# Performance work log

Measured on AMD Instinct MI355X. Metric: run time of the kernel, lower is better.

The kernel has to match this reference:

```python
import jax, jax.numpy as jnp
import numpy as np

N = 100000
E = 1000000
IN_F, HID, NCLS = 128, 128, 40
EPS = 1e-5


def _gconv(h, src, dst, W, b):
    # DGL GraphConv with norm='both', allow_zero_in_degree=True (degrees clamped to >=1).
    ones = jnp.ones(src.shape, jnp.float32)
    dout = jnp.clip(jax.ops.segment_sum(ones, src, num_segments=N), 1.0)   # out-degree of src nodes
    din = jnp.clip(jax.ops.segment_sum(ones, dst, num_segments=N), 1.0)    # in-degree of dst nodes
    x = (h * jax.lax.rsqrt(dout)[:, None]) @ W            # [N, out] matmul-first (linear commutes with sum-aggregation)
    y = jax.ops.segment_sum(x[src], dst, num_segments=N)  # SpMM: scatter-add over edges
    y = y * jax.lax.rsqrt(din)[:, None]
    return y + b if b is not None else y


def _bn(h, gamma, beta):
    # BatchNorm1d training-mode math over the node dimension (biased variance).
    m = jnp.mean(h, axis=0)
    v = jnp.mean(jnp.square(h - m), axis=0)
    return (h - m) * jax.lax.rsqrt(v + EPS) * gamma + beta


def setup_inputs() -> dict:
    key = jax.random.key(0)
    ks = jax.random.split(key, 16)
    feat = jax.random.normal(ks[0], (N, IN_F), jnp.float32)
    src0 = jax.random.randint(ks[1], (E,), 0, N, jnp.int32)
    dst0 = jax.random.randint(ks[2], (E,), 0, N, jnp.int32)
    src1 = jax.random.randint(ks[3], (E,), 0, N, jnp.int32)
    dst1 = jax.random.randint(ks[4], (E,), 0, N, jnp.int32)
    order_attn = jax.random.uniform(ks[5], (2,), jnp.float32)
    s = lambda d_in, d_out: 1.0 / np.sqrt(d_in)
    W0 = jax.random.uniform(ks[6], (IN_F, HID), jnp.float32, -s(IN_F, HID), s(IN_F, HID))
    W1 = jax.random.uniform(ks[7], (HID, HID), jnp.float32, -s(HID, HID), s(HID, HID))
    W2 = jax.random.uniform(ks[8], (HID, NCLS), jnp.float32, -s(HID, NCLS), s(HID, NCLS))
    b2 = jnp.zeros((NCLS,), jnp.float32)
    L0 = jax.random.uniform(ks[9], (IN_F, HID), jnp.float32, -s(IN_F, HID), s(IN_F, HID))
    L1 = jax.random.uniform(ks[10], (HID, HID), jnp.float32, -s(HID, HID), s(HID, HID))
    L2 = jax.random.uniform(ks[11], (HID, NCLS), jnp.float32, -s(HID, NCLS), s(HID, NCLS))
    gamma0 = jnp.ones((HID,), jnp.float32); beta0 = jnp.zeros((HID,), jnp.float32)
    gamma1 = jnp.ones((HID,), jnp.float32); beta1 = jnp.zeros((HID,), jnp.float32)
    return dict(feat=feat, src0=src0, dst0=dst0, src1=src1, dst1=dst1, order_attn=order_attn,
                W0=W0, W1=W1, W2=W2, b2=b2, L0=L0, L1=L1, L2=L2,
                gamma0=gamma0, beta0=beta0, gamma1=gamma1, beta1=beta1)


def reference(feat, src0, dst0, src1, dst1, order_attn, W0, W1, W2, b2, L0, L1, L2,
              gamma0, beta0, gamma1, beta1):
    # Multi-graph path (len(graph)==2, n_layers==3, use_linear=True); dropout = identity (eval).
    h = feat
    # layer 0: order_attn-weighted combination of two adjacency variants
    conv1 = _gconv(h, src0, dst0, W0, None)
    conv2 = _gconv(h, src1, dst1, W0, None)
    conv = order_attn[0] * conv1 + order_attn[1] * conv2
    h = conv + h @ L0
    h = jax.nn.relu(_bn(h, gamma0, beta0))
    # layer 1 (convs[-2]) on graph[0]
    h = _gconv(h, src0, dst0, W1, None) + h @ L1
    h = jax.nn.relu(_bn(h, gamma1, beta1))
    # layer 2 (convs[-1]) on graph[0], with bias
    h = _gconv(h, src0, dst0, W2, b2) + h @ L2
    return h
```

## Files before the change

kernel.cpp:

```cpp
#include <hip/hip_runtime.h>
#include <math.h>

#define N_NODES 100000
#define N_EDGES 1000000
#define F 128
#define NC 40
#define BN_EPS 1e-5f
#define CH 32
#define EC (N_EDGES / CH)
#define WIN0 65536
#define NB1 (N_NODES - WIN0)
#define PROW (N_NODES / 4)

typedef unsigned int uint;
typedef unsigned short ushort;
typedef __attribute__((ext_vector_type(8))) short vbf8;
typedef __attribute__((ext_vector_type(4))) float vf4;

__device__ __forceinline__ float bf_lo(uint v) { return __uint_as_float(v << 16); }
__device__ __forceinline__ float bf_hi(uint v) { return __uint_as_float(v & 0xffff0000u); }
__device__ __forceinline__ ushort f2bf(float f) {
  uint u = __float_as_uint(f);
  u = u + 0x7fffu + ((u >> 16) & 1u);
  return (ushort)(u >> 16);
}
__device__ __forceinline__ uint pk2(float a, float b) {
  return (uint)f2bf(a) | ((uint)f2bf(b) << 16);
}

__global__ __launch_bounds__(256) void hist_count_k(
    const int* __restrict__ s0, const int* __restrict__ d0,
    const int* __restrict__ s1, const int* __restrict__ d1,
    unsigned* __restrict__ partial) {
  __shared__ unsigned bins[16384];
  int c = blockIdx.x, w = blockIdx.y, a = blockIdx.z;
  const int* keys = (a == 0) ? s0 : (a == 1) ? d0 : (a == 2) ? s1 : d1;
  int base = w * WIN0;
  int nb = w ? NB1 : WIN0;
  int nwords = nb >> 2;
  int t = threadIdx.x;
  for (int i = t; i < nwords; i += 256) bins[i] = 0;
  __syncthreads();
  int e0 = c * EC;
  for (int e = e0 + t; e < e0 + EC; e += 256) {
    int b = keys[e] - base;
    if ((unsigned)b < (unsigned)nb)
      atomicAdd(&bins[b >> 2], 1u << ((b & 3) * 8));
  }
  __syncthreads();
  unsigned* dst = partial + (size_t)(a * CH + c) * PROW + (w ? (WIN0 >> 2) : 0);
  for (int i = t; i < nwords; i += 256) dst[i] = bins[i];
}

__global__ __launch_bounds__(256) void deg_reduce_k(
    unsigned* __restrict__ partial, float* __restrict__ rs4, ushort* __restrict__ rsO01u,
    int* __restrict__ degIn0, int* __restrict__ degIn1,
    float* __restrict__ st0, float* __restrict__ st1) {
  int word = blockIdx.x * 256 + threadIdx.x;
  if (blockIdx.y == 0 && word < 256) { st0[word] = 0.f; st1[word] = 0.f; }
  if (word >= PROW) return;
  int a = blockIdx.y;
  bool din = (a == 1) || (a == 3);
  unsigned r0 = 0, r1 = 0, r2 = 0, r3 = 0;
  unsigned* rowp = partial + (size_t)a * CH * PROW + word;
  for (int c = 0; c < CH; ++c) {
    unsigned* p = rowp + (size_t)c * PROW;
    unsigned v = *p;
    if (din) *p = r0 | (r1 << 8) | (r2 << 16) | (r3 << 24);
    r0 += v & 255u; r1 += (v >> 8) & 255u; r2 += (v >> 16) & 255u; r3 += (v >> 24) & 255u;
  }
  int b = word * 4;
  float4 r;
  r.x = rsqrtf((float)max(r0, 1u));
  r.y = rsqrtf((float)max(r1, 1u));
  r.z = rsqrtf((float)max(r2, 1u));
  r.w = rsqrtf((float)max(r3, 1u));
  *(float4*)&rs4[(size_t)a * N_NODES + b] = r;
  if (a == 0) {
    rsO01u[2 * (b + 0)] = f2bf(r.x); rsO01u[2 * (b + 1)] = f2bf(r.y);
    rsO01u[2 * (b + 2)] = f2bf(r.z); rsO01u[2 * (b + 3)] = f2bf(r.w);
  }
  if (a == 2) {
    rsO01u[2 * (b + 0) + 1] = f2bf(r.x); rsO01u[2 * (b + 1) + 1] = f2bf(r.y);
    rsO01u[2 * (b + 2) + 1] = f2bf(r.z); rsO01u[2 * (b + 3) + 1] = f2bf(r.w);
  }
  if (a == 1) { degIn0[b] = r0; degIn0[b + 1] = r1; degIn0[b + 2] = r2; degIn0[b + 3] = r3; }
  if (a == 3) { degIn1[b] = r0; degIn1[b + 1] = r1; degIn1[b + 2] = r2; degIn1[b + 3] = r3; }
}

__global__ void scan_local_k(const int* __restrict__ cnt0, const int* __restrict__ cnt1,
                             int* __restrict__ out0, int* __restrict__ out1,
                             int* __restrict__ bsum) {
  __shared__ int lds[256];
  const int* cnt = blockIdx.y ? cnt1 : cnt0;
  int* out = blockIdx.y ? out1 : out0;
  int base = blockIdx.x * 2048;
  int t = threadIdx.x;
  int v[8];
  int s = 0;
#pragma unroll
  for (int j = 0; j < 8; ++j) {
    int idx = base + t * 8 + j;
    v[j] = (idx < N_NODES) ? cnt[idx] : 0;
    s += v[j];
  }
  lds[t] = s;
  __syncthreads();
  for (int off = 1; off < 256; off <<= 1) {
    int x = (t >= off) ? lds[t - off] : 0;
    __syncthreads();
    lds[t] += x;
    __syncthreads();
  }
  int excl = lds[t] - s;
  if (t == 255) bsum[blockIdx.y * 64 + blockIdx.x] = lds[255];
  int run = excl;
#pragma unroll
  for (int j = 0; j < 8; ++j) {
    int idx = base + t * 8 + j;
    if (idx < N_NODES) out[idx] = run;
    run += v[j];
  }
}

__global__ void scan_top_k(int* bsum, int nb) {
  int w = threadIdx.x >> 6, t = threadIdx.x & 63;
  int* b = bsum + w * 64;
  int orig = (t < nb) ? b[t] : 0;
  int v = orig;
  for (int off = 1; off < 64; off <<= 1) {
    int u = __shfl_up(v, off);
    if (t >= off) v += u;
  }
  if (t < nb) b[t] = v - orig;
}

__global__ void scan_apply_k(int* __restrict__ rp0, int* __restrict__ rp1,
                             const int* __restrict__ bsum) {
  int* rp = blockIdx.y ? rp1 : rp0;
  const int* bs = bsum + blockIdx.y * 64;
  int i = blockIdx.x * 256 + threadIdx.x;
  if (i < N_NODES) rp[i] += bs[i >> 11];
  if (i == 0) rp[N_NODES] = N_EDGES;
}

__global__ __launch_bounds__(256) void csr_fill2_k(
    const int* __restrict__ src0, const int* __restrict__ dst0, const int* __restrict__ rp0g,
    int* __restrict__ csr0g,
    const int* __restrict__ src1, const int* __restrict__ dst1, const int* __restrict__ rp1g,
    int* __restrict__ csr1g, const unsigned* __restrict__ partial) {
  __shared__ unsigned bins[16384];
  int c = blockIdx.x, w = blockIdx.y, g = blockIdx.z;
  const int* src = g ? src1 : src0;
  const int* dst = g ? dst1 : dst0;
  const int* rp = g ? rp1g : rp0g;
  int* csr = g ? csr1g : csr0g;
  int aIdx = g ? 3 : 1;
  int base = w * WIN0;
  int nb = w ? NB1 : WIN0;
  int nwords = nb >> 2;
  const unsigned* sp = partial + (size_t)(aIdx * CH + c) * PROW + (w ? (WIN0 >> 2) : 0);
  int t = threadIdx.x;
  for (int i = t; i < nwords; i += 256) bins[i] = sp[i];
  __syncthreads();
  int e0 = c * EC;
  for (int e = e0 + t; e < e0 + EC; e += 256) {
    int d = dst[e];
    int b = d - base;
    if ((unsigned)b < (unsigned)nb) {
      int sh = (b & 3) * 8;
      unsigned old = atomicAdd(&bins[b >> 2], 1u << sh);
      int off = (old >> sh) & 255;
      csr[rp[d] + off] = src[e];
    }
  }
}

__global__ __launch_bounds__(256) void pack_all_k(
    const float* __restrict__ x, uint* __restrict__ y,
    const float* __restrict__ Wa, const float* __restrict__ Wb,
    const float* __restrict__ Wc, const float* __restrict__ Wd,
    ushort* __restrict__ pk) {
  int b = blockIdx.x;
  int t = threadIdx.x;
  if (b < 1024) {
    size_t total = (size_t)N_NODES * F / 8;
    for (size_t idx = b * 256 + t; idx < total; idx += (size_t)1024 * 256) {
      float4 v1 = ((const float4*)x)[idx * 2];
      float4 v2 = ((const float4*)x)[idx * 2 + 1];
      uint4 o;
      o.x = pk2(v1.x, v1.y);
      o.y = pk2(v1.z, v1.w);
      o.z = pk2(v2.x, v2.y);
      o.w = pk2(v2.z, v2.w);
      ((uint4*)y)[idx] = o;
    }
  } else {
    int bb = b - 1024;
    int m = bb >> 3;
    int idx = (bb & 7) * 256 + t;
    const float* W = (m == 0) ? Wa : (m == 1) ? Wb : (m == 2) ? Wc : Wd;
    int lane = idx & 63;
    int nt = (idx >> 6) & 7;
    int ks = idx >> 9;
    int j = (lane & 15) + nt * 16;
    int kb = (lane >> 4) * 8 + ks * 32;
    ushort v[8];
#pragma unroll
    for (int q = 0; q < 8; ++q) v[q] = f2bf(W[(size_t)(kb + q) * F + j]);
    *(uint4*)(pk + (size_t)m * 16384 + (size_t)idx * 8) = *(uint4*)v;
  }
}

__device__ __forceinline__ void acc8(uint4 v, float c, float* a) {
  a[0] = fmaf(bf_lo(v.x), c, a[0]); a[1] = fmaf(bf_hi(v.x), c, a[1]);
  a[2] = fmaf(bf_lo(v.y), c, a[2]); a[3] = fmaf(bf_hi(v.y), c, a[3]);
  a[4] = fmaf(bf_lo(v.z), c, a[4]); a[5] = fmaf(bf_hi(v.z), c, a[5]);
  a[6] = fmaf(bf_lo(v.w), c, a[6]); a[7] = fmaf(bf_hi(v.w), c, a[7]);
}

__device__ __forceinline__ void gather_run(const int* __restrict__ p, int n, float w,
                                           const float* __restrict__ rsO,
                                           const uint4* __restrict__ xr, int l, float* a) {
  int e = 0;
  for (; e + 3 < n; e += 4) {
    int s0 = p[e], s1 = p[e + 1], s2 = p[e + 2], s3 = p[e + 3];
    float c0 = w * rsO[s0], c1 = w * rsO[s1];
    float c2 = w * rsO[s2], c3 = w * rsO[s3];
    uint4 v0 = xr[(size_t)s0 * 16 + l];
    uint4 v1 = xr[(size_t)s1 * 16 + l];
    uint4 v2 = xr[(size_t)s2 * 16 + l];
    uint4 v3 = xr[(size_t)s3 * 16 + l];
    acc8(v0, c0, a); acc8(v1, c1, a); acc8(v2, c2, a); acc8(v3, c3, a);
  }
  for (; e < n; ++e) {
    int s = p[e];
    float c = w * rsO[s];
    uint4 v = xr[(size_t)s * 16 + l];
    acc8(v, c, a);
  }
}

__global__ __launch_bounds__(256) void gather_dual_q_k(
    const uint* __restrict__ xbf, const float* __restrict__ attn,
    const float* __restrict__ rsO0f, const float* __restrict__ rsO1f,
    const float* __restrict__ rsI0, const int* __restrict__ rp0, const int* __restrict__ csr0,
    const float* __restrict__ rsI1, const int* __restrict__ rp1, const int* __restrict__ csr1,
    uint* __restrict__ outbf) {
  int node = blockIdx.x * 16 + (threadIdx.x >> 4);
  int l = threadIdx.x & 15;
  int b0 = rp0[node], n0 = rp0[node + 1] - b0;
  int b1 = rp1[node], n1 = rp1[node + 1] - b1;
  float w0 = attn[0] * rsI0[node];
  float w1 = attn[1] * rsI1[node];
  const uint4* xr = (const uint4*)xbf;
  float a[8] = {0.f, 0.f, 0.f, 0.f, 0.f, 0.f, 0.f, 0.f};
  gather_run(csr0 + b0, n0, w0, rsO0f, xr, l, a);
  gather_run(csr1 + b1, n1, w1, rsO1f, xr, l, a);
  uint4 o;
  o.x = pk2(a[0], a[1]); o.y = pk2(a[2], a[3]);
  o.z = pk2(a[4], a[5]); o.w = pk2(a[6], a[7]);
  ((uint4*)outbf)[(size_t)node * 16 + l] = o;
}

__device__ __forceinline__ void accbn(uint4 v, float c, const float* sc, const float* sh,
                                      float* a) {
  a[0] = fmaf(fmaxf(fmaf(bf_lo(v.x), sc[0], sh[0]), 0.f), c, a[0]);
  a[1] = fmaf(fmaxf(fmaf(bf_hi(v.x), sc[1], sh[1]), 0.f), c, a[1]);
  a[2] = fmaf(fmaxf(fmaf(bf_lo(v.y), sc[2], sh[2]), 0.f), c, a[2]);
  a[3] = fmaf(fmaxf(fmaf(bf_hi(v.y), sc[3], sh[3]), 0.f), c, a[3]);
  a[4] = fmaf(fmaxf(fmaf(bf_lo(v.z), sc[4], sh[4]), 0.f), c, a[4]);
  a[5] = fmaf(fmaxf(fmaf(bf_hi(v.z), sc[5], sh[5]), 0.f), c, a[5]);
  a[6] = fmaf(fmaxf(fmaf(bf_lo(v.w), sc[6], sh[6]), 0.f), c, a[6]);
  a[7] = fmaf(fmaxf(fmaf(bf_hi(v.w), sc[7], sh[7]), 0.f), c, a[7]);
}

__global__ __launch_bounds__(256) void gather_bn_q_k(
    const uint* __restrict__ xbf, const float* __restrict__ st,
    const float* __restrict__ gamma, const float* __restrict__ beta,
    const float* __restrict__ rsO,
    const float* __restrict__ rsI, const int* __restrict__ rp, const int* __restrict__ csr,
    uint* __restrict__ outbf) {
  int node = blockIdx.x * 16 + (threadIdx.x >> 4);
  int l = threadIdx.x & 15;
  float sc[8], sh[8];
#pragma unroll
  for (int j = 0; j < 8; ++j) {
    int c = 8 * l + j;
    float m = st[c] * (1.f / (float)N_NODES);
    float v = st[128 + c] * (1.f / (float)N_NODES) - m * m;
    float s = gamma[c] * rsqrtf(fmaxf(v, 0.f) + BN_EPS);
    sc[j] = s;
    sh[j] = beta[c] - m * s;
  }
  int b0 = rp[node], T = rp[node + 1] - b0;
  const int* p = csr + b0;
  const uint4* xr = (const uint4*)xbf;
  float a[8] = {0.f, 0.f, 0.f, 0.f, 0.f, 0.f, 0.f, 0.f};
  int e = 0;
  for (; e + 1 < T; e += 2) {
    int s0 = p[e], s1 = p[e + 1];
    float c0 = rsO[s0], c1 = rsO[s1];
    uint4 v0 = xr[(size_t)s0 * 16 + l];
    uint4 v1 = xr[(size_t)s1 * 16 + l];
    accbn(v0, c0, sc, sh, a);
    accbn(v1, c1, sc, sh, a);
  }
  if (e < T) {
    int s0 = p[e];
    float c0 = rsO[s0];
    uint4 v0 = xr[(size_t)s0 * 16 + l];
    accbn(v0, c0, sc, sh, a);
  }
  float sd = rsI[node];
  uint4 o;
  o.x = pk2(a[0] * sd, a[1] * sd); o.y = pk2(a[2] * sd, a[3] * sd);
  o.z = pk2(a[4] * sd, a[5] * sd); o.w = pk2(a[6] * sd, a[7] * sd);
  ((uint4*)outbf)[(size_t)node * 16 + l] = o;
}

__global__ void gather40_add_k(const uint* __restrict__ x2bf, const float* __restrict__ rsI,
                               const int* __restrict__ rp, const int* __restrict__ csr,
                               float* __restrict__ out) {
  int node = (blockIdx.x * 256 + threadIdx.x) >> 5;
  int lane = threadIdx.x & 31;
  if (node >= N_NODES || lane >= 20) return;
  float l = 0.f, h = 0.f;
  int e = rp[node], end = rp[node + 1];
  for (; e + 3 < end; e += 4) {
    int sA = csr[e], sB = csr[e + 1], sC = csr[e + 2], sD = csr[e + 3];
    uint vA = x2bf[(size_t)sA * 20 + lane];
    uint vB = x2bf[(size_t)sB * 20 + lane];
    uint vC = x2bf[(size_t)sC * 20 + lane];
    uint vD = x2bf[(size_t)sD * 20 + lane];
    l += (bf_lo(vA) + bf_lo(vB)) + (bf_lo(vC) + bf_lo(vD));
    h += (bf_hi(vA) + bf_hi(vB)) + (bf_hi(vC) + bf_hi(vD));
  }
  for (; e < end; ++e) {
    uint vA = x2bf[(size_t)csr[e] * 20 + lane];
    l += bf_lo(vA);
    h += bf_hi(vA);
  }
  float sd = rsI[node];
  float2 p = *(float2*)(out + (size_t)node * NC + lane * 2);
  *(float2*)(out + (size_t)node * NC + lane * 2) = make_float2(p.x + l * sd, p.y + h * sd);
}

__global__ __launch_bounds__(256) void gemm_mfma_k(
    const ushort* __restrict__ A1, const ushort* __restrict__ A2,
    const ushort* __restrict__ pkA, const ushort* __restrict__ pkB,
    float* __restrict__ st, ushort* __restrict__ Cb) {
  __shared__ float sst[256];
  int t = threadIdx.x;
  int wave = t >> 6, lane = t & 63;
  int kgrp = lane >> 4, lrow = lane & 15;
  int arow = blockIdx.x * 64 + wave * 16 + lrow;
  bool rok = arow < N_NODES;
  const vbf8* a1p = (const vbf8*)(A1 + (size_t)(rok ? arow : 0) * F);
  const vbf8* a2p = (const vbf8*)(A2 + (size_t)(rok ? arow : 0) * F);
  const vbf8* wap = (const vbf8*)pkA + lane;
  const vbf8* wbp = (const vbf8*)pkB + lane;
  sst[t] = 0.f;
  __syncthreads();
  vbf8 zero = {0, 0, 0, 0, 0, 0, 0, 0};
  vf4 acc[8];
#pragma unroll
  for (int i = 0; i < 8; ++i) acc[i] = (vf4){0.f, 0.f, 0.f, 0.f};
#pragma unroll
  for (int ks = 0; ks < 4; ++ks) {
    vbf8 a1 = rok ? a1p[ks * 4 + kgrp] : zero;
    vbf8 a2 = rok ? a2p[ks * 4 + kgrp] : zero;
#pragma unroll
    for (int nt = 0; nt < 8; ++nt)
      acc[nt] = __builtin_amdgcn_mfma_f32_16x16x32_bf16(a1, wap[(ks * 8 + nt) * 64], acc[nt], 0, 0, 0);
#pragma unroll
    for (int nt = 0; nt < 8; ++nt)
      acc[nt] = __builtin_amdgcn_mfma_f32_16x16x32_bf16(a2, wbp[(ks * 8 + nt) * 64], acc[nt], 0, 0, 0);
  }
  int rbase = blockIdx.x * 64 + wave * 16 + kgrp * 4;
#pragma unroll
  for (int nt = 0; nt < 8; ++nt) {
    int col = nt * 16 + lrow;
#pragma unroll
    for (int r = 0; r < 4; ++r) {
      int row = rbase + r;
      if (row < N_NODES) Cb[(size_t)row * F + col] = f2bf(acc[nt][r]);
    }
  }
#pragma unroll
  for (int nt = 0; nt < 8; ++nt) {
    float s = acc[nt][0] + acc[nt][1] + acc[nt][2] + acc[nt][3];
    float q = acc[nt][0] * acc[nt][0] + acc[nt][1] * acc[nt][1] +
              acc[nt][2] * acc[nt][2] + acc[nt][3] * acc[nt][3];
    s += __shfl_xor(s, 16); q += __shfl_xor(q, 16);
    s += __shfl_xor(s, 32); q += __shfl_xor(q, 32);
    if (lane < 16) {
      atomicAdd(&sst[nt * 16 + lane], s);
      atomicAdd(&sst[128 + nt * 16 + lane], q);
    }
  }
  __syncthreads();
  atomicAdd(&st[t], sst[t]);
}

__global__ __launch_bounds__(256) void gemm_mfma_bn_k(
    const ushort* __restrict__ A1, const ushort* __restrict__ A2,
    const float* __restrict__ stin, const float* __restrict__ gamma,
    const float* __restrict__ beta,
    const ushort* __restrict__ pkA, const ushort* __restrict__ pkB,
    float* __restrict__ st, ushort* __restrict__ Cb) {
  __shared__ float sst[256];
  __shared__ float scl[128], shl[128];
  int t = threadIdx.x;
  int wave = t >> 6, lane = t & 63;
  int kgrp = lane >> 4, lrow = lane & 15;
  int arow = blockIdx.x * 64 + wave * 16 + lrow;
  bool rok = arow < N_NODES;
  if (t < 128) {
    float m = stin[t] * (1.f / (float)N_NODES);
    float v = stin[128 + t] * (1.f / (float)N_NODES) - m * m;
    float s = gamma[t] * rsqrtf(fmaxf(v, 0.f) + BN_EPS);
    scl[t] = s;
    shl[t] = beta[t] - m * s;
  }
  const vbf8* a1p = (const vbf8*)(A1 + (size_t)(rok ? arow : 0) * F);
  const vbf8* a2p = (const vbf8*)(A2 + (size_t)(rok ? arow : 0) * F);
  const vbf8* wap = (const vbf8*)pkA + lane;
  const vbf8* wbp = (const vbf8*)pkB + lane;
  sst[t] = 0.f;
  __syncthreads();
  vbf8 zero = {0, 0, 0, 0, 0, 0, 0, 0};
  vf4 acc[8];
#pragma unroll
  for (int i = 0; i < 8; ++i) acc[i] = (vf4){0.f, 0.f, 0.f, 0.f};
#pragma unroll
  for (int ks = 0; ks < 4; ++ks) {
    vbf8 a1 = rok ? a1p[ks * 4 + kgrp] : zero;
    vbf8 a2 = zero;
    if (rok) {
      vbf8 a2r = a2p[ks * 4 + kgrp];
      const float* scp = &scl[ks * 32 + kgrp * 8];
      const float* shp = &shl[ks * 32 + kgrp * 8];
      ushort o[8];
#pragma unroll
      for (int q = 0; q < 8; ++q) {
        float f = __uint_as_float(((uint)(ushort)a2r[q]) << 16);
        f = fmaxf(fmaf(f, scp[q], shp[q]), 0.f);
        o[q] = f2bf(f);
      }
      a2 = *(vbf8*)o;
    }
#pragma unroll
    for (int nt = 0; nt < 8; ++nt)
      acc[nt] = __builtin_amdgcn_mfma_f32_16x16x32_bf16(a1, wap[(ks * 8 + nt) * 64], acc[nt], 0, 0, 0);
#pragma unroll
    for (int nt = 0; nt < 8; ++nt)
      acc[nt] = __builtin_amdgcn_mfma_f32_16x16x32_bf16(a2, wbp[(ks * 8 + nt) * 64], acc[nt], 0, 0, 0);
  }
  int rbase = blockIdx.x * 64 + wave * 16 + kgrp * 4;
#pragma unroll
  for (int nt = 0; nt < 8; ++nt) {
    int col = nt * 16 + lrow;
#pragma unroll
    for (int r = 0; r < 4; ++r) {
      int row = rbase + r;
      if (row < N_NODES) Cb[(size_t)row * F + col] = f2bf(acc[nt][r]);
    }
  }
#pragma unroll
  for (int nt = 0; nt < 8; ++nt) {
    float s = acc[nt][0] + acc[nt][1] + acc[nt][2] + acc[nt][3];
    float q = acc[nt][0] * acc[nt][0] + acc[nt][1] * acc[nt][1] +
              acc[nt][2] * acc[nt][2] + acc[nt][3] * acc[nt][3];
    s += __shfl_xor(s, 16); q += __shfl_xor(q, 16);
    s += __shfl_xor(s, 32); q += __shfl_xor(q, 32);
    if (lane < 16) {
      atomicAdd(&sst[nt * 16 + lane], s);
      atomicAdd(&sst[128 + nt * 16 + lane], q);
    }
  }
  __syncthreads();
  atomicAdd(&st[t], sst[t]);
}

__global__ __launch_bounds__(256) void gemm40_dual_k(
    const uint* __restrict__ h1b, const float* __restrict__ st,
    const float* __restrict__ gamma, const float* __restrict__ beta,
    const float* __restrict__ W2, const float* __restrict__ L2, const float* __restrict__ bias,
    const float* __restrict__ rsO, uint* __restrict__ x2bf, float* __restrict__ outp) {
  __shared__ float Alds[25 * 128];
  __shared__ float Wl[128 * NC];
  __shared__ float Ll[128 * NC];
  __shared__ float scl[128], shl[128];
  int t = threadIdx.x;
  int r0 = blockIdx.x * 25;
  if (t < 128) {
    float m = st[t] / (float)N_NODES;
    float v = st[128 + t] / (float)N_NODES - m * m;
    float s = gamma[t] * rsqrtf(fmaxf(v, 0.f) + BN_EPS);
    scl[t] = s;
    shl[t] = beta[t] - m * s;
  }
  __syncthreads();
#pragma unroll
  for (int p = 0; p < 4; ++p) {
    int flat = t * 4 + p * 1024;
    if (flat < 25 * 128) {
      int lrr = flat >> 7, k = flat & 127;
      int row = r0 + lrr;
      float4 v = make_float4(0.f, 0.f, 0.f, 0.f);
      if (row < N_NODES) {
        uint2 u = *(const uint2*)(h1b + (size_t)row * 64 + (k >> 1));
        v = make_float4(bf_lo(u.x), bf_hi(u.x), bf_lo(u.y), bf_hi(u.y));
      }
      float4 scv = *(float4*)&scl[k];
      float4 shv = *(float4*)&shl[k];
      v.x = fmaxf(fmaf(v.x, scv.x, shv.x), 0.f);
      v.y = fmaxf(fmaf(v.y, scv.y, shv.y), 0.f);
      v.z = fmaxf(fmaf(v.z, scv.z, shv.z), 0.f);
      v.w = fmaxf(fmaf(v.w, scv.w, shv.w), 0.f);
      *(float4*)&Alds[flat] = v;
    }
  }
#pragma unroll
  for (int p = 0; p < 5; ++p) {
    int flat = t * 4 + p * 1024;
    if (flat < 128 * NC) {
      *(float4*)&Wl[flat] = *(const float4*)(W2 + flat);
      *(float4*)&Ll[flat] = *(const float4*)(L2 + flat);
    }
  }
  __syncthreads();
  if (t < 250) {
    int lrr = t / 10, cg = t % 10;
    float w0 = 0.f, w1 = 0.f, w2 = 0.f, w3 = 0.f;
    float l0 = 0.f, l1 = 0.f, l2 = 0.f, l3 = 0.f;
#pragma unroll 8
    for (int k = 0; k < 128; ++k) {
      float a = Alds[lrr * 128 + k];
      float4 w = *(float4*)&Wl[k * NC + cg * 4];
      float4 l = *(float4*)&Ll[k * NC + cg * 4];
      w0 = fmaf(a, w.x, w0); w1 = fmaf(a, w.y, w1);
      w2 = fmaf(a, w.z, w2); w3 = fmaf(a, w.w, w3);
      l0 = fmaf(a, l.x, l0); l1 = fmaf(a, l.y, l1);
      l2 = fmaf(a, l.z, l2); l3 = fmaf(a, l.w, l3);
    }
    int row = r0 + lrr;
    if (row < N_NODES) {
      float s = rsO[row];
      uint2 xo = make_uint2(pk2(w0 * s, w1 * s), pk2(w2 * s, w3 * s));
      *(uint2*)(x2bf + (size_t)row * 20 + cg * 2) = xo;
      float4 bv = *(const float4*)(bias + cg * 4);
      float4 oo = make_float4(l0 + bv.x, l1 + bv.y, l2 + bv.z, l3 + bv.w);
      *(float4*)(outp + (size_t)row * NC + cg * 4) = oo;
    }
  }
}

extern "C" void kernel_launch(void* const* d_in, const int* in_sizes, int n_in,
                              void* d_out, int out_size, void* d_ws, size_t ws_size,
                              hipStream_t stream) {
  const float* feat = (const float*)d_in[0];
  const int* src0 = (const int*)d_in[1];
  const int* dst0 = (const int*)d_in[2];
  const int* src1 = (const int*)d_in[3];
  const int* dst1 = (const int*)d_in[4];
  const float* attn = (const float*)d_in[5];
  const float* W0 = (const float*)d_in[6];
  const float* W1 = (const float*)d_in[7];
  const float* W2 = (const float*)d_in[8];
  const float* b2 = (const float*)d_in[9];
  const float* L0 = (const float*)d_in[10];
  const float* L1 = (const float*)d_in[11];
  const float* L2 = (const float*)d_in[12];
  const float* gamma0 = (const float*)d_in[13];
  const float* beta0 = (const float*)d_in[14];
  const float* gamma1 = (const float*)d_in[15];
  const float* beta1 = (const float*)d_in[16];
  float* out = (float*)d_out;

  char* base = (char*)d_ws;
  size_t off = 0;
  auto alloc = [&](size_t bytes) -> void* {
    void* p = base + off;
    off += (bytes + 255) & ~(size_t)255;
    return p;
  };
  unsigned* partial = (unsigned*)alloc((size_t)4 * CH * PROW * 4);
  float* rs4 = (float*)alloc(4 * (size_t)N_NODES * 4);
  uint* rsO01 = (uint*)alloc((size_t)N_NODES * 4);
  int* degIn0 = (int*)alloc(N_NODES * 4);
  int* degIn1 = (int*)alloc(N_NODES * 4);
  int* rp0 = (int*)alloc((N_NODES + 1) * 4);
  int* rp1 = (int*)alloc((N_NODES + 1) * 4);
  int* bsum = (int*)alloc(128 * 4);
  int* csr0 = (int*)alloc((size_t)N_EDGES * 4);
  int* csr1 = (int*)alloc((size_t)N_EDGES * 4);
  float* st0 = (float*)alloc(256 * 4);
  float* st1 = (float*)alloc(256 * 4);
  ushort* wpk = (ushort*)alloc((size_t)4 * 16384 * 2);
  uint* featbf = (uint*)alloc((size_t)N_NODES * 64 * 4);
  uint* aggbf = (uint*)alloc((size_t)N_NODES * 64 * 4);
  uint* hrow = (uint*)alloc((size_t)N_NODES * 64 * 4);
  uint* g1buf = (uint*)alloc((size_t)N_NODES * 64 * 4);
  if (off > ws_size) return;

  uint* x2bf = featbf;

  float* rs_out0 = rs4;
  float* rs_in0 = rs4 + N_NODES;
  float* rs_out1 = rs4 + 2 * N_NODES;
  float* rs_in1 = rs4 + 3 * N_NODES;

  hist_count_k<<<dim3(CH, 2, 4), 256, 0, stream>>>(src0, dst0, src1, dst1, partial);
  deg_reduce_k<<<dim3((PROW + 255) / 256, 4), 256, 0, stream>>>(
      partial, rs4, (ushort*)rsO01, degIn0, degIn1, st0, st1);
  const int SCB = (N_NODES + 2047) / 2048;
  scan_local_k<<<dim3(SCB, 2), 256, 0, stream>>>(degIn0, degIn1, rp0, rp1, bsum);
  scan_top_k<<<1, 128, 0, stream>>>(bsum, SCB);
  scan_apply_k<<<dim3((N_NODES + 255) / 256, 2), 256, 0, stream>>>(rp0, rp1, bsum);
  csr_fill2_k<<<dim3(CH, 2, 2), 256, 0, stream>>>(src0, dst0, rp0, csr0,
                                                  src1, dst1, rp1, csr1, partial);

  pack_all_k<<<1056, 256, 0, stream>>>(feat, featbf, W0, L0, W1, L1, wpk);

  const int GB = (N_NODES + 63) / 64;

  gather_dual_q_k<<<N_NODES / 16, 256, 0, stream>>>(featbf, attn, rs_out0, rs_out1,
                                                    rs_in0, rp0, csr0,
                                                    rs_in1, rp1, csr1, aggbf);
  gemm_mfma_k<<<GB, 256, 0, stream>>>((ushort*)aggbf, (ushort*)featbf, wpk, wpk + 16384,
                                      st0, (ushort*)hrow);

  gather_bn_q_k<<<N_NODES / 16, 256, 0, stream>>>(hrow, st0, gamma0, beta0, rs_out0,
                                                  rs_in0, rp0, csr0, g1buf);
  gemm_mfma_bn_k<<<GB, 256, 0, stream>>>((ushort*)g1buf, (ushort*)hrow, st0, gamma0, beta0,
                                         wpk + 2 * 16384, wpk + 3 * 16384, st1, (ushort*)hrow);

  gemm40_dual_k<<<(N_NODES + 24) / 25, 256, 0, stream>>>(hrow, st1, gamma1, beta1, W2, L2, b2,
                                                         rs_out0, x2bf, out);
  gather40_add_k<<<(N_NODES * 32 + 255) / 256, 256, 0, stream>>>(x2bf, rs_in0, rp0, csr0, out);
}
```

Before: 492.5 us.

## Fuse SpMM gathers into MFMA GEMM kernels via LDS-staged A tiles

Merges the neighbor-gather kernels into the following MFMA GEMM kernels for layers 0 and 1. Each block gathers the aggregated rows for its 64 nodes into padded shared memory and feeds them straight to the MFMA loop. This removes the aggregated-feature buffer write and reread and cuts two launches. In exchange, each block now does 4 nodes per 16-lane group serially, so there is less parallelism and latency hiding in the gather phase, plus extra LDS use that may lower occupancy. Layer 1 output now goes to a separate buffer instead of being written in place.

Result: no change. 489.8 us (-0.5%).

```diff
diff --git a/kernel.cpp b/kernel.cpp
--- a/kernel.cpp
+++ b/kernel.cpp
@@ -11,6 +11,7 @@
 #define WIN0 65536
 #define NB1 (N_NODES - WIN0)
 #define PROW (N_NODES / 4)
+#define ALD 66
 
 typedef unsigned int uint;
 typedef unsigned short ushort;
@@ -241,28 +242,6 @@
   }
 }
 
-__global__ __launch_bounds__(256) void gather_dual_q_k(
-    const uint* __restrict__ xbf, const float* __restrict__ attn,
-    const float* __restrict__ rsO0f, const float* __restrict__ rsO1f,
-    const float* __restrict__ rsI0, const int* __restrict__ rp0, const int* __restrict__ csr0,
-    const float* __restrict__ rsI1, const int* __restrict__ rp1, const int* __restrict__ csr1,
-    uint* __restrict__ outbf) {
-  int node = blockIdx.x * 16 + (threadIdx.x >> 4);
-  int l = threadIdx.x & 15;
-  int b0 = rp0[node], n0 = rp0[node + 1] - b0;
-  int b1 = rp1[node], n1 = rp1[node + 1] - b1;
-  float w0 = attn[0] * rsI0[node];
-  float w1 = attn[1] * rsI1[node];
-  const uint4* xr = (const uint4*)xbf;
-  float a[8] = {0.f, 0.f, 0.f, 0.f, 0.f, 0.f, 0.f, 0.f};
-  gather_run(csr0 + b0, n0, w0, rsO0f, xr, l, a);
-  gather_run(csr1 + b1, n1, w1, rsO1f, xr, l, a);
-  uint4 o;
-  o.x = pk2(a[0], a[1]); o.y = pk2(a[2], a[3]);
-  o.z = pk2(a[4], a[5]); o.w = pk2(a[6], a[7]);
-  ((uint4*)outbf)[(size_t)node * 16 + l] = o;
-}
-
 __device__ __forceinline__ void accbn(uint4 v, float c, const float* sc, const float* sh,
                                       float* a) {
   a[0] = fmaf(fmaxf(fmaf(bf_lo(v.x), sc[0], sh[0]), 0.f), c, a[0]);
@@ -273,50 +252,6 @@
   a[5] = fmaf(fmaxf(fmaf(bf_hi(v.z), sc[5], sh[5]), 0.f), c, a[5]);
   a[6] = fmaf(fmaxf(fmaf(bf_lo(v.w), sc[6], sh[6]), 0.f), c, a[6]);
   a[7] = fmaf(fmaxf(fmaf(bf_hi(v.w), sc[7], sh[7]), 0.f), c, a[7]);
-}
-
-__global__ __launch_bounds__(256) void gather_bn_q_k(
-    const uint* __restrict__ xbf, const float* __restrict__ st,
-    const float* __restrict__ gamma, const float* __restrict__ beta,
-    const float* __restrict__ rsO,
-    const float* __restrict__ rsI, const int* __restrict__ rp, const int* __restrict__ csr,
-    uint* __restrict__ outbf) {
-  int node = blockIdx.x * 16 + (threadIdx.x >> 4);
-  int l = threadIdx.x & 15;
-  float sc[8], sh[8];
-#pragma unroll
-  for (int j = 0; j < 8; ++j) {
-    int c = 8 * l + j;
-    float m = st[c] * (1.f / (float)N_NODES);
-    float v = st[128 + c] * (1.f / (float)N_NODES) - m * m;
-    float s = gamma[c] * rsqrtf(fmaxf(v, 0.f) + BN_EPS);
-    sc[j] = s;
-    sh[j] = beta[c] - m * s;
-  }
-  int b0 = rp[node], T = rp[node + 1] - b0;
-  const int* p = csr + b0;
-  const uint4* xr = (const uint4*)xbf;
-  float a[8] = {0.f, 0.f, 0.f, 0.f, 0.f, 0.f, 0.f, 0.f};
-  int e = 0;
-  for (; e + 1 < T; e += 2) {
-    int s0 = p[e], s1 = p[e + 1];
-    float c0 = rsO[s0], c1 = rsO[s1];
-    uint4 v0 = xr[(size_t)s0 * 16 + l];
-    uint4 v1 = xr[(size_t)s1 * 16 + l];
-    accbn(v0, c0, sc, sh, a);
-    accbn(v1, c1, sc, sh, a);
-  }
-  if (e < T) {
-    int s0 = p[e];
-    float c0 = rsO[s0];
-    uint4 v0 = xr[(size_t)s0 * 16 + l];
-    accbn(v0, c0, sc, sh, a);
-  }
-  float sd = rsI[node];
-  uint4 o;
-  o.x = pk2(a[0] * sd, a[1] * sd); o.y = pk2(a[2] * sd, a[3] * sd);
-  o.z = pk2(a[4] * sd, a[5] * sd); o.w = pk2(a[6] * sd, a[7] * sd);
-  ((uint4*)outbf)[(size_t)node * 16 + l] = o;
 }
 
 __global__ void gather40_add_k(const uint* __restrict__ x2bf, const float* __restrict__ rsI,
@@ -346,29 +281,53 @@
   *(float2*)(out + (size_t)node * NC + lane * 2) = make_float2(p.x + l * sd, p.y + h * sd);
 }
 
-__global__ __launch_bounds__(256) void gemm_mfma_k(
-    const ushort* __restrict__ A1, const ushort* __restrict__ A2,
+__global__ __launch_bounds__(256) void gemm_g_mfma_k(
+    const uint* __restrict__ xbf, const float* __restrict__ attn,
+    const float* __restrict__ rsO0f, const float* __restrict__ rsO1f,
+    const float* __restrict__ rsI0, const int* __restrict__ rp0, const int* __restrict__ csr0,
+    const float* __restrict__ rsI1, const int* __restrict__ rp1, const int* __restrict__ csr1,
     const ushort* __restrict__ pkA, const ushort* __restrict__ pkB,
     float* __restrict__ st, ushort* __restrict__ Cb) {
+  __shared__ uint Alds[64 * ALD];
   __shared__ float sst[256];
   int t = threadIdx.x;
+  sst[t] = 0.f;
+  {
+    int g = t >> 4, l = t & 15;
+    const uint4* xr = (const uint4*)xbf;
+    float w0 = attn[0], w1 = attn[1];
+#pragma unroll
+    for (int i = 0; i < 4; ++i) {
+      int ln = g * 4 + i;
+      int node = blockIdx.x * 64 + ln;
+      float a[8] = {0.f, 0.f, 0.f, 0.f, 0.f, 0.f, 0.f, 0.f};
+      if (node < N_NODES) {
+        int b0 = rp0[node], n0 = rp0[node + 1] - b0;
+        int b1 = rp1[node], n1 = rp1[node + 1] - b1;
+        gather_run(csr0 + b0, n0, w0 * rsI0[node], rsO0f, xr, l, a);
+        gather_run(csr1 + b1, n1, w1 * rsI1[node], rsO1f, xr, l, a);
+      }
+      uint4 o;
+      o.x = pk2(a[0], a[1]); o.y = pk2(a[2], a[3]);
+      o.z = pk2(a[4], a[5]); o.w = pk2(a[6], a[7]);
+      *(uint4*)&Alds[ln * ALD + l * 4] = o;
+    }
+  }
+  __syncthreads();
   int wave = t >> 6, lane = t & 63;
   int kgrp = lane >> 4, lrow = lane & 15;
   int arow = blockIdx.x * 64 + wave * 16 + lrow;
   bool rok = arow < N_NODES;
-  const vbf8* a1p = (const vbf8*)(A1 + (size_t)(rok ? arow : 0) * F);
-  const vbf8* a2p = (const vbf8*)(A2 + (size_t)(rok ? arow : 0) * F);
+  const vbf8* a2p = (const vbf8*)((const ushort*)xbf + (size_t)(rok ? arow : 0) * F);
   const vbf8* wap = (const vbf8*)pkA + lane;
   const vbf8* wbp = (const vbf8*)pkB + lane;
-  sst[t] = 0.f;
-  __syncthreads();
   vbf8 zero = {0, 0, 0, 0, 0, 0, 0, 0};
   vf4 acc[8];
 #pragma unroll
   for (int i = 0; i < 8; ++i) acc[i] = (vf4){0.f, 0.f, 0.f, 0.f};
 #pragma unroll
   for (int ks = 0; ks < 4; ++ks) {
-    vbf8 a1 = rok ? a1p[ks * 4 + kgrp] : zero;
+    vbf8 a1 = *(const vbf8*)&Alds[(wave * 16 + lrow) * ALD + (ks * 4 + kgrp) * 4];
     vbf8 a2 = rok ? a2p[ks * 4 + kgrp] : zero;
 #pragma unroll
     for (int nt = 0; nt < 8; ++nt)
@@ -403,19 +362,19 @@
   atomicAdd(&st[t], sst[t]);
 }
 
-__global__ __launch_bounds__(256) void gemm_mfma_bn_k(
-    const ushort* __restrict__ A1, const ushort* __restrict__ A2,
+__global__ __launch_bounds__(256) void gemm_g_bn_k(
+    const uint* __restrict__ xbf,
     const float* __restrict__ stin, const float* __restrict__ gamma,
     const float* __restrict__ beta,
+    const float* __restrict__ rsO,
+    const float* __restrict__ rsI, const int* __restrict__ rp, const int* __restrict__ csr,
     const ushort* __restrict__ pkA, const ushort* __restrict__ pkB,
     float* __restrict__ st, ushort* __restrict__ Cb) {
+  __shared__ uint Alds[64 * ALD];
   __shared__ float sst[256];
   __shared__ float scl[128], shl[128];
   int t = threadIdx.x;
-  int wave = t >> 6, lane = t & 63;
-  int kgrp = lane >> 4, lrow = lane & 15;
-  int arow = blockIdx.x * 64 + wave * 16 + lrow;
-  bool rok = arow < N_NODES;
+  sst[t] = 0.f;
   if (t < 128) {
     float m = stin[t] * (1.f / (float)N_NODES);
     float v = stin[128 + t] * (1.f / (float)N_NODES) - m * m;
@@ -423,19 +382,60 @@
     scl[t] = s;
     shl[t] = beta[t] - m * s;
   }
-  const vbf8* a1p = (const vbf8*)(A1 + (size_t)(rok ? arow : 0) * F);
-  const vbf8* a2p = (const vbf8*)(A2 + (size_t)(rok ? arow : 0) * F);
+  __syncthreads();
+  {
+    int g = t >> 4, l = t & 15;
+    const uint4* xr = (const uint4*)xbf;
+    float sc[8], sh[8];
+#pragma unroll
+    for (int j = 0; j < 8; ++j) { sc[j] = scl[8 * l + j]; sh[j] = shl[8 * l + j]; }
+#pragma unroll
+    for (int i = 0; i < 4; ++i) {
+      int ln = g * 4 + i;
+      int node = blockIdx.x * 64 + ln;
+      float a[8] = {0.f, 0.f, 0.f, 0.f, 0.f, 0.f, 0.f, 0.f};
+      float sd = 0.f;
+      if (node < N_NODES) {
+        sd = rsI[node];
+        int b0 = rp[node], T = rp[node + 1] - b0;
+        const int* p = csr + b0;
+        int e = 0;
+        for (; e + 1 < T; e += 2) {
+          int s0 = p[e], s1 = p[e + 1];
+          float c0 = rsO[s0], c1 = rsO[s1];
+          uint4 v0 = xr[(size_t)s0 * 16 + l];
+          uint4 v1 = xr[(size_t)s1 * 16 + l];
+          accbn(v0, c0, sc, sh, a);
+          accbn(v1, c1, sc, sh, a);
+        }
+        if (e < T) {
+          int s0 = p[e];
+          float c0 = rsO[s0];
+          uint4 v0 = xr[(size_t)s0 * 16 + l];
+          accbn(v0, c0, sc, sh, a);
+        }
+      }
+      uint4 o;
+      o.x = pk2(a[0] * sd, a[1] * sd); o.y = pk2(a[2] * sd, a[3] * sd);
+      o.z = pk2(a[4] * sd, a[5] * sd); o.w = pk2(a[6] * sd, a[7] * sd);
+      *(uint4*)&Alds[ln * ALD + l * 4] = o;
+    }
+  }
+  __syncthreads();
+  int wave = t >> 6, lane = t & 63;
+  int kgrp = lane >> 4, lrow = lane & 15;
+  int arow = blockIdx.x * 64 + wave * 16 + lrow;
+  bool rok = arow < N_NODES;
+  const vbf8* a2p = (const vbf8*)((const ushort*)xbf + (size_t)(rok ? arow : 0) * F);
   const vbf8* wap = (const vbf8*)pkA + lane;
   const vbf8* wbp = (const vbf8*)pkB + lane;
-  sst[t] = 0.f;
-  __syncthreads();
   vbf8 zero = {0, 0, 0, 0, 0, 0, 0, 0};
   vf4 acc[8];
 #pragma unroll
   for (int i = 0; i < 8; ++i) acc[i] = (vf4){0.f, 0.f, 0.f, 0.f};
 #pragma unroll
   for (int ks = 0; ks < 4; ++ks) {
-    vbf8 a1 = rok ? a1p[ks * 4 + kgrp] : zero;
+    vbf8 a1 = *(const vbf8*)&Alds[(wave * 16 + lrow) * ALD + (ks * 4 + kgrp) * 4];
     vbf8 a2 = zero;
     if (rok) {
       vbf8 a2r = a2p[ks * 4 + kgrp];
@@ -600,7 +600,6 @@
   float* st1 = (float*)alloc(256 * 4);
   ushort* wpk = (ushort*)alloc((size_t)4 * 16384 * 2);
   uint* featbf = (uint*)alloc((size_t)N_NODES * 64 * 4);
-  uint* aggbf = (uint*)alloc((size_t)N_NODES * 64 * 4);
   uint* hrow = (uint*)alloc((size_t)N_NODES * 64 * 4);
   uint* g1buf = (uint*)alloc((size_t)N_NODES * 64 * 4);
   if (off > ws_size) return;
@@ -626,18 +625,15 @@
 
   const int GB = (N_NODES + 63) / 64;
 
-  gather_dual_q_k<<<N_NODES / 16, 256, 0, stream>>>(featbf, attn, rs_out0, rs_out1,
-                                                    rs_in0, rp0, csr0,
-                                                    rs_in1, rp1, csr1, aggbf);
-  gemm_mfma_k<<<GB, 256, 0, stream>>>((ushort*)aggbf, (ushort*)featbf, wpk, wpk + 16384,
-                                      st0, (ushort*)hrow);
-
-  gather_bn_q_k<<<N_NODES / 16, 256, 0, stream>>>(hrow, st0, gamma0, beta0, rs_out0,
-                                                  rs_in0, rp0, csr0, g1buf);
-  gemm_mfma_bn_k<<<GB, 256, 0, stream>>>((ushort*)g1buf, (ushort*)hrow, st0, gamma0, beta0,
-                                         wpk + 2 * 16384, wpk + 3 * 16384, st1, (ushort*)hrow);
-
-  gemm40_dual_k<<<(N_NODES + 24) / 25, 256, 0, stream>>>(hrow, st1, gamma1, beta1, W2, L2, b2,
+  gemm_g_mfma_k<<<GB, 256, 0, stream>>>(featbf, attn, rs_out0, rs_out1,
+                                        rs_in0, rp0, csr0, rs_in1, rp1, csr1,
+                                        wpk, wpk + 16384, st0, (ushort*)hrow);
+
+  gemm_g_bn_k<<<GB, 256, 0, stream>>>(hrow, st0, gamma0, beta0, rs_out0,
+                                      rs_in0, rp0, csr0,
+                                      wpk + 2 * 16384, wpk + 3 * 16384, st1, (ushort*)g1buf);
+
+  gemm40_dual_k<<<(N_NODES + 24) / 25, 256, 0, stream>>>(g1buf, st1, gamma1, beta1, W2, L2, b2,
                                                          rs_out0, x2bf, out);
   gather40_add_k<<<(N_NODES * 32 + 255) / 256, 256, 0, stream>>>(x2bf, rs_in0, rp0, csr0, out);
 }
```

## Stage GEMM outputs in LDS for coalesced stores; replace BN-stat atomics with two-stage reduction

Applied to the files above, without the earlier changes.

Both MFMA GEMM kernels now pack pairs of bf16 results through a lane shuffle into a padded LDS tile, then write each 64-row block with coalesced 16-byte stores instead of scattered 2-byte stores. The per-block BatchNorm sum and sum-of-squares partials are written to a per-block buffer rather than atomically added into one 256-float array. Two small kernels then reduce those partials deterministically. This removes global atomic contention and uncoalesced writes, at the cost of extra LDS use, two more launches per layer, and an extra partial buffer.

New measurement: 468.1 us. -5.0%, faster.

```diff
diff --git a/kernel.cpp b/kernel.cpp
--- a/kernel.cpp
+++ b/kernel.cpp
@@ -11,6 +11,8 @@
 #define WIN0 65536
 #define NB1 (N_NODES - WIN0)
 #define PROW (N_NODES / 4)
+#define CSU 68
+#define GB 1563
 
 typedef unsigned int uint;
 typedef unsigned short ushort;
@@ -54,10 +56,8 @@
 
 __global__ __launch_bounds__(256) void deg_reduce_k(
     unsigned* __restrict__ partial, float* __restrict__ rs4, ushort* __restrict__ rsO01u,
-    int* __restrict__ degIn0, int* __restrict__ degIn1,
-    float* __restrict__ st0, float* __restrict__ st1) {
+    int* __restrict__ degIn0, int* __restrict__ degIn1) {
   int word = blockIdx.x * 256 + threadIdx.x;
-  if (blockIdx.y == 0 && word < 256) { st0[word] = 0.f; st1[word] = 0.f; }
   if (word >= PROW) return;
   int a = blockIdx.y;
   bool din = (a == 1) || (a == 3);
@@ -210,6 +210,22 @@
     for (int q = 0; q < 8; ++q) v[q] = f2bf(W[(size_t)(kb + q) * F + j]);
     *(uint4*)(pk + (size_t)m * 16384 + (size_t)idx * 8) = *(uint4*)v;
   }
+}
+
+__global__ void st_part_k(const float* __restrict__ stm, float* __restrict__ stp, int ncopies) {
+  int b = blockIdx.x, t = threadIdx.x;
+  int lo = b * 25, hi = min(ncopies, lo + 25);
+  float s = 0.f;
+  for (int k = lo; k < hi; ++k) s += stm[(size_t)k * 256 + t];
+  stp[b * 256 + t] = s;
+}
+
+__global__ void st_final_k(const float* __restrict__ stp, float* __restrict__ st) {
+  int t = threadIdx.x;
+  float s = 0.f;
+#pragma unroll
+  for (int k = 0; k < 64; ++k) s += stp[k * 256 + t];
+  st[t] = s;
 }
 
 __device__ __forceinline__ void acc8(uint4 v, float c, float* a) {
@@ -349,9 +365,12 @@
 __global__ __launch_bounds__(256) void gemm_mfma_k(
     const ushort* __restrict__ A1, const ushort* __restrict__ A2,
     const ushort* __restrict__ pkA, const ushort* __restrict__ pkB,
-    float* __restrict__ st, ushort* __restrict__ Cb) {
+    float* __restrict__ stm, ushort* __restrict__ Cb) {
+  __shared__ uint Cl[64 * CSU];
   __shared__ float sst[256];
   int t = threadIdx.x;
+  sst[t] = 0.f;
+  __syncthreads();
   int wave = t >> 6, lane = t & 63;
   int kgrp = lane >> 4, lrow = lane & 15;
   int arow = blockIdx.x * 64 + wave * 16 + lrow;
@@ -360,8 +379,6 @@
   const vbf8* a2p = (const vbf8*)(A2 + (size_t)(rok ? arow : 0) * F);
   const vbf8* wap = (const vbf8*)pkA + lane;
   const vbf8* wbp = (const vbf8*)pkB + lane;
-  sst[t] = 0.f;
-  __syncthreads();
   vbf8 zero = {0, 0, 0, 0, 0, 0, 0, 0};
   vf4 acc[8];
 #pragma unroll
@@ -377,14 +394,14 @@
     for (int nt = 0; nt < 8; ++nt)
       acc[nt] = __builtin_amdgcn_mfma_f32_16x16x32_bf16(a2, wbp[(ks * 8 + nt) * 64], acc[nt], 0, 0, 0);
   }
-  int rbase = blockIdx.x * 64 + wave * 16 + kgrp * 4;
+  int row_l = wave * 16 + kgrp * 4;
 #pragma unroll
   for (int nt = 0; nt < 8; ++nt) {
-    int col = nt * 16 + lrow;
 #pragma unroll
     for (int r = 0; r < 4; ++r) {
-      int row = rbase + r;
-      if (row < N_NODES) Cb[(size_t)row * F + col] = f2bf(acc[nt][r]);
+      float w = acc[nt][r];
+      float o = __shfl_xor(w, 1);
+      if ((lrow & 1) == 0) Cl[(row_l + r) * CSU + nt * 8 + (lrow >> 1)] = pk2(w, o);
     }
   }
 #pragma unroll
@@ -400,7 +417,15 @@
     }
   }
   __syncthreads();
-  atomicAdd(&st[t], sst[t]);
+#pragma unroll
+  for (int i = 0; i < 4; ++i) {
+    int u = t + 256 * i;
+    int row = u >> 4, seg = (u & 15) * 4;
+    int grow = blockIdx.x * 64 + row;
+    if (grow < N_NODES)
+      *(uint4*)((uint*)Cb + (size_t)grow * 64 + seg) = *(uint4*)&Cl[row * CSU + seg];
+  }
+  stm[(size_t)blockIdx.x * 256 + t] = sst[t];
 }
 
 __global__ __launch_bounds__(256) void gemm_mfma_bn_k(
@@ -408,14 +433,12 @@
     const float* __restrict__ stin, const float* __restrict__ gamma,
     const float* __restrict__ beta,
     const ushort* __restrict__ pkA, const ushort* __restrict__ pkB,
-    float* __restrict__ st, ushort* __restrict__ Cb) {
+    float* __restrict__ stm, ushort* __restrict__ Cb) {
+  __shared__ uint Cl[64 * CSU];
   __shared__ float sst[256];
   __shared__ float scl[128], shl[128];
   int t = threadIdx.x;
-  int wave = t >> 6, lane = t & 63;
-  int kgrp = lane >> 4, lrow = lane & 15;
-  int arow = blockIdx.x * 64 + wave * 16 + lrow;
-  bool rok = arow < N_NODES;
+  sst[t] = 0.f;
   if (t < 128) {
     float m = stin[t] * (1.f / (float)N_NODES);
     float v = stin[128 + t] * (1.f / (float)N_NODES) - m * m;
@@ -423,12 +446,15 @@
     scl[t] = s;
     shl[t] = beta[t] - m * s;
   }
+  __syncthreads();
+  int wave = t >> 6, lane = t & 63;
+  int kgrp = lane >> 4, lrow = lane & 15;
+  int arow = blockIdx.x * 64 + wave * 16 + lrow;
+  bool rok = arow < N_NODES;
   const vbf8* a1p = (const vbf8*)(A1 + (size_t)(rok ? arow : 0) * F);
   const vbf8* a2p = (const vbf8*)(A2 + (size_t)(rok ? arow : 0) * F);
   const vbf8* wap = (const vbf8*)pkA + lane;
   const vbf8* wbp = (const vbf8*)pkB + lane;
-  sst[t] = 0.f;
-  __syncthreads();
   vbf8 zero = {0, 0, 0, 0, 0, 0, 0, 0};
   vf4 acc[8];
 #pragma unroll
@@ -457,14 +483,14 @@
     for (int nt = 0; nt < 8; ++nt)
       acc[nt] = __builtin_amdgcn_mfma_f32_16x16x32_bf16(a2, wbp[(ks * 8 + nt) * 64], acc[nt], 0, 0, 0);
   }
-  int rbase = blockIdx.x * 64 + wave * 16 + kgrp * 4;
+  int row_l = wave * 16 + kgrp * 4;
 #pragma unroll
   for (int nt = 0; nt < 8; ++nt) {
-    int col = nt * 16 + lrow;
 #pragma unroll
     for (int r = 0; r < 4; ++r) {
-      int row = rbase + r;
-      if (row < N_NODES) Cb[(size_t)row * F + col] = f2bf(acc[nt][r]);
+      float w = acc[nt][r];
+      float o = __shfl_xor(w, 1);
+      if ((lrow & 1) == 0) Cl[(row_l + r) * CSU + nt * 8 + (lrow >> 1)] = pk2(w, o);
     }
   }
 #pragma unroll
@@ -480,7 +506,15 @@
     }
   }
   __syncthreads();
-  atomicAdd(&st[t], sst[t]);
+#pragma unroll
+  for (int i = 0; i < 4; ++i) {
+    int u = t + 256 * i;
+    int row = u >> 4, seg = (u & 15) * 4;
+    int grow = blockIdx.x * 64 + row;
+    if (grow < N_NODES)
+      *(uint4*)((uint*)Cb + (size_t)grow * 64 + seg) = *(uint4*)&Cl[row * CSU + seg];
+  }
+  stm[(size_t)blockIdx.x * 256 + t] = sst[t];
 }
 
 __global__ __launch_bounds__(256) void gemm40_dual_k(
@@ -596,6 +630,9 @@
   int* bsum = (int*)alloc(128 * 4);
   int* csr0 = (int*)alloc((size_t)N_EDGES * 4);
   int* csr1 = (int*)alloc((size_t)N_EDGES * 4);
+  float* stm0 = (float*)alloc((size_t)GB * 256 * 4);
+  float* stm1 = (float*)alloc((size_t)GB * 256 * 4);
+  float* stp = (float*)alloc((size_t)64 * 256 * 4);
   float* st0 = (float*)alloc(256 * 4);
   float* st1 = (float*)alloc(256 * 4);
   ushort* wpk = (ushort*)alloc((size_t)4 * 16384 * 2);
@@ -614,7 +651,7 @@
 
   hist_count_k<<<dim3(CH, 2, 4), 256, 0, stream>>>(src0, dst0, src1, dst1, partial);
   deg_reduce_k<<<dim3((PROW + 255) / 256, 4), 256, 0, stream>>>(
-      partial, rs4, (ushort*)rsO01, degIn0, degIn1, st0, st1);
+      partial, rs4, (ushort*)rsO01, degIn0, degIn1);
   const int SCB = (N_NODES + 2047) / 2048;
   scan_local_k<<<dim3(SCB, 2), 256, 0, stream>>>(degIn0, degIn1, rp0, rp1, bsum);
   scan_top_k<<<1, 128, 0, stream>>>(bsum, SCB);
@@ -624,18 +661,20 @@
 
   pack_all_k<<<1056, 256, 0, stream>>>(feat, featbf, W0, L0, W1, L1, wpk);
 
-  const int GB = (N_NODES + 63) / 64;
-
   gather_dual_q_k<<<N_NODES / 16, 256, 0, stream>>>(featbf, attn, rs_out0, rs_out1,
                                                     rs_in0, rp0, csr0,
                                                     rs_in1, rp1, csr1, aggbf);
   gemm_mfma_k<<<GB, 256, 0, stream>>>((ushort*)aggbf, (ushort*)featbf, wpk, wpk + 16384,
-                                      st0, (ushort*)hrow);
+                                      stm0, (ushort*)hrow);
+  st_part_k<<<64, 256, 0, stream>>>(stm0, stp, GB);
+  st_final_k<<<1, 256, 0, stream>>>(stp, st0);
 
   gather_bn_q_k<<<N_NODES / 16, 256, 0, stream>>>(hrow, st0, gamma0, beta0, rs_out0,
                                                   rs_in0, rp0, csr0, g1buf);
   gemm_mfma_bn_k<<<GB, 256, 0, stream>>>((ushort*)g1buf, (ushort*)hrow, st0, gamma0, beta0,
-                                         wpk + 2 * 16384, wpk + 3 * 16384, st1, (ushort*)hrow);
+                                         wpk + 2 * 16384, wpk + 3 * 16384, stm1, (ushort*)hrow);
+  st_part_k<<<64, 256, 0, stream>>>(stm1, stp, GB);
+  st_final_k<<<1, 256, 0, stream>>>(stp, st1);
 
   gemm40_dual_k<<<(N_NODES + 24) / 25, 256, 0, stream>>>(hrow, st1, gamma1, beta1, W2, L2, b2,
                                                          rs_out0, x2bf, out);
```
